# Performance work log

Hardware: AMD Instinct MI355X
Metric: run time of the kernel (lower is better)

The kernel has to match this reference:

```python
import jax, jax.numpy as jnp
import numpy as np

DEPTH, DIM, HEADS, MLP_HID, POS_DIM, PROJ_DIM, NCLS, INP = 5, 128, 8, 256, 128, 128, 1000, 35
EPS = 1e-5

def _ln(x, g, b):
    m = x.mean(-1, keepdims=True)
    v = ((x - m) ** 2).mean(-1, keepdims=True)
    return (x - m) / jnp.sqrt(v + EPS) * g + b

def _gelu(x):
    return jax.nn.gelu(x, approximate=False)  # torch nn.GELU default (erf)

def setup_inputs() -> dict:
    key = jax.random.key(0)
    ks = iter(jax.random.split(key, 80))
    nxt = lambda: next(ks)
    B, N = 8, 1024
    w = lambda *s: (jax.random.normal(nxt(), s, jnp.float32) / np.sqrt(s[-2]).astype(np.float32))
    z = lambda *s: jnp.zeros(s, jnp.float32)
    o = lambda *s: jnp.ones(s, jnp.float32)
    node_feat = jax.random.normal(nxt(), (B, N, 3), jnp.float32)
    a = (jax.random.uniform(nxt(), (B, N, N)) < 0.01).astype(jnp.float32)
    adj = jnp.maximum(a, a.transpose(0, 2, 1))  # symmetric 0/1 adjacency
    lapl = jax.random.normal(nxt(), (B, N, 32), jnp.float32) * 0.1
    d = dict(
        node_feat=node_feat, adj=adj, lapl=lapl,
        cls_token=jax.random.normal(nxt(), (1, 1, DIM), jnp.float32),
        pe_w1=w(INP, 2 * INP), pe_b1=z(2 * INP),
        pe_w2=w(2 * INP, 2 * INP), pe_b2=z(2 * INP),
        pe_w3=w(2 * INP, 2 * INP), pe_b3=z(2 * INP),
        pe_lng=o(2 * INP), pe_lnb=z(2 * INP),
        pe_w4=w(2 * INP, POS_DIM), pe_b4=z(POS_DIM),
        blk_ln1_g=o(DEPTH, DIM), blk_ln1_b=z(DEPTH, DIM),
        blk_qkv_w=w(DEPTH, DIM, 3 * HEADS * DIM),
        blk_proj_w=w(DEPTH, HEADS * DIM, DIM), blk_proj_b=z(DEPTH, DIM),
        blk_gamma_w=jax.random.uniform(nxt(), (DEPTH, DIM, 2), jnp.float32) * 0.01,
        blk_gamma_b=z(DEPTH, 2),
        blk_ln2_g=o(DEPTH, DIM), blk_ln2_b=z(DEPTH, DIM),
        blk_mlp_w1=w(DEPTH, DIM, MLP_HID), blk_mlp_b1=z(DEPTH, MLP_HID),
        blk_mlp_w2=w(DEPTH, MLP_HID, DIM), blk_mlp_b2=z(DEPTH, DIM),
        head_lng=o(DIM), head_lnb=z(DIM), head_w=w(DIM, DIM), head_b=z(DIM),
        proj_w1=w(DIM, PROJ_DIM), proj_b1=z(PROJ_DIM),
        proj_w2=w(PROJ_DIM, PROJ_DIM), proj_b2=z(PROJ_DIM),
        proj_w3=w(PROJ_DIM, PROJ_DIM), proj_b3=z(PROJ_DIM),
        proj_lng=o(PROJ_DIM), proj_lnb=z(PROJ_DIM),
        proj_w4=w(PROJ_DIM, NCLS), proj_b4=z(NCLS),
    )
    return d

def reference(node_feat, adj, lapl, cls_token, pe_w1, pe_b1, pe_w2, pe_b2, pe_w3, pe_b3,
              pe_lng, pe_lnb, pe_w4, pe_b4, blk_ln1_g, blk_ln1_b, blk_qkv_w, blk_proj_w,
              blk_proj_b, blk_gamma_w, blk_gamma_b, blk_ln2_g, blk_ln2_b, blk_mlp_w1,
              blk_mlp_b1, blk_mlp_w2, blk_mlp_b2, head_lng, head_lnb, head_w, head_b,
              proj_w1, proj_b1, proj_w2, proj_b2, proj_w3, proj_b3, proj_lng, proj_lnb,
              proj_w4, proj_b4):
    B, N, _ = node_feat.shape
    M = N + 1
    # positional-encoding MLP on concatenated [node_feat | lapl] (inp_dim = 35)
    x = jnp.concatenate([node_feat, lapl], axis=2)
    x = _gelu(x @ pe_w1 + pe_b1)
    x = _gelu(x @ pe_w2 + pe_b2)
    x = _gelu(x @ pe_w3 + pe_b3)
    x = _ln(x, pe_lng, pe_lnb) @ pe_w4 + pe_b4  # [B,N,DIM]
    x = jnp.concatenate([jnp.broadcast_to(cls_token, (B, 1, DIM)), x], axis=1)  # [B,M,DIM]
    # adjacency with cls row/col, adj_cls[:,0,0] = 1
    adj_cls = jnp.zeros((B, M, M), x.dtype).at[:, 0, 0].set(1.0).at[:, 1:, 1:].set(adj)
    scale = DIM ** (-0.5)
    for i in range(DEPTH):
        h = _ln(x, blk_ln1_g[i], blk_ln1_b[i])
        qkv = (h @ blk_qkv_w[i]).reshape(B, M, 3, HEADS, DIM).transpose(2, 0, 3, 1, 4)
        q, k, v = qkv[0], qkv[1], qkv[2]  # each [B,H,M,D]
        attn = jnp.einsum('bhnd,bhmd->bhnm', q, k) * scale
        gamma = jnp.exp(h @ blk_gamma_w[i] + blk_gamma_b[i])  # [B,M,2], use_exp=True
        attn = gamma[:, None, :, 0:1] * attn + gamma[:, None, :, 1:2] * adj_cls[:, None]
        attn = jax.nn.softmax(attn, axis=-1)
        o = jnp.einsum('bhnm,bhmd->bhnd', attn, v).transpose(0, 2, 1, 3).reshape(B, M, HEADS * DIM)
        x = o @ blk_proj_w[i] + blk_proj_b[i] + h  # residual from normed input (as in source)
        h2 = _ln(x, blk_ln2_g[i], blk_ln2_b[i])
        x = _gelu(h2 @ blk_mlp_w1[i] + blk_mlp_b1[i]) @ blk_mlp_w2[i] + blk_mlp_b2[i] + h2
    c = x[:, 0]
    c = _ln(c, head_lng, head_lnb) @ head_w + head_b  # mlp_head
    p = _gelu(c @ proj_w1 + proj_b1)
    p = _gelu(p @ proj_w2 + proj_b2)
    p = _gelu(p @ proj_w3 + proj_b3)
    p = _ln(p, proj_lng, proj_lnb) @ proj_w4 + proj_b4
    return (c, p)
```

## Files before the change

kernel.cpp:

```cpp
#include <hip/hip_runtime.h>
#include <hip/hip_bf16.h>
#include <math.h>

#define NB 8
#define NSEQ 1024
#define M_ 1025
#define ROWS (NB * M_)
#define DIMC 128
#define NHEADS 8
#define QKV3 3072
#define PEROWS (NB * NSEQ)
#define ACS 1088

typedef __attribute__((ext_vector_type(8))) short bf16x8;
typedef __attribute__((ext_vector_type(4))) float f32x4;

__device__ __forceinline__ float gelu_f(float x) {
  return 0.5f * x * (1.f + erff(x * 0.70710678118654752440f));
}

__device__ __forceinline__ unsigned short f2bf(float f) {
  __hip_bfloat16 h = __float2bfloat16(f);
  return *reinterpret_cast<unsigned short*>(&h);
}

__device__ __forceinline__ float bf2f(unsigned short u) {
  union { unsigned int i; float f; } c;
  c.i = ((unsigned int)u) << 16;
  return c.f;
}

template<int TR>
__global__ __launch_bounds__(256) void rowgemm_k(
    const float* __restrict__ in, const float* __restrict__ W,
    const float* __restrict__ bias, const float* __restrict__ res,
    float* __restrict__ out, int rows, int K, int Nout, int act, int remap)
{
  extern __shared__ float s_in[];
  const int tid = threadIdx.x;
  const int r0 = blockIdx.x * TR;
  const int tot = TR * K;
  for (int idx = tid; idx < tot; idx += blockDim.x) {
    int r = idx / K;
    int k = idx - r * K;
    int gr = r0 + r;
    s_in[idx] = (gr < rows) ? in[(size_t)gr * K + k] : 0.f;
  }
  __syncthreads();
  const int j = blockIdx.y * blockDim.x + tid;
  if (j >= Nout) return;
  float acc[TR];
  const float bv = bias ? bias[j] : 0.f;
#pragma unroll
  for (int r = 0; r < TR; ++r) acc[r] = bv;
  for (int k = 0; k < K; ++k) {
    const float w = W[(size_t)k * Nout + j];
#pragma unroll
    for (int r = 0; r < TR; ++r) acc[r] = fmaf(s_in[r * K + k], w, acc[r]);
  }
  for (int r = 0; r < TR; ++r) {
    const int gr = r0 + r;
    if (gr >= rows) break;
    float v = acc[r];
    if (act == 1) v = gelu_f(v);
    if (res) v += res[(size_t)gr * Nout + j];
    const size_t orow = remap ? (size_t)(gr + gr / 1024 + 1) : (size_t)gr;
    out[orow * (size_t)Nout + j] = v;
  }
}

template<int ACT, int OBF, int RES>
__global__ __launch_bounds__(256) void mgemm_k(
    const unsigned short* __restrict__ Xb, const unsigned short* __restrict__ Wt,
    const float* __restrict__ bias, const float* __restrict__ res,
    void* __restrict__ outp, int rows, int K, int N)
{
  __shared__ unsigned short sX[64][72];
  __shared__ unsigned short sW[64][72];
  const int tid = threadIdx.x;
  const int w = tid >> 6, lane = tid & 63;
  const int col = lane & 15, quad = lane >> 4;
  const int r0 = blockIdx.x * 64, n0 = blockIdx.y * 64;
  const int lr = tid >> 2, lc = tid & 3;
  const int xrow = min(r0 + lr, rows - 1);
  const unsigned short* xsrc = Xb + (size_t)xrow * K + lc * 8;
  const unsigned short* wsrc = Wt + (size_t)(n0 + lr) * K + lc * 8;

  f32x4 acc[4];
#pragma unroll
  for (int t = 0; t < 4; ++t) acc[t] = (f32x4){0.f, 0.f, 0.f, 0.f};

  for (int k0 = 0; k0 < K; k0 += 64) {
    __syncthreads();
    *(uint4*)&sX[lr][lc * 8]      = *(const uint4*)(xsrc + k0);
    *(uint4*)&sX[lr][lc * 8 + 32] = *(const uint4*)(xsrc + k0 + 32);
    *(uint4*)&sW[lr][lc * 8]      = *(const uint4*)(wsrc + k0);
    *(uint4*)&sW[lr][lc * 8 + 32] = *(const uint4*)(wsrc + k0 + 32);
    __syncthreads();
    const bf16x8 aX0 = *(const bf16x8*)&sX[w * 16 + col][quad * 8];
    const bf16x8 aX1 = *(const bf16x8*)&sX[w * 16 + col][32 + quad * 8];
#pragma unroll
    for (int t = 0; t < 4; ++t) {
      const bf16x8 bW0 = *(const bf16x8*)&sW[t * 16 + col][quad * 8];
      const bf16x8 bW1 = *(const bf16x8*)&sW[t * 16 + col][32 + quad * 8];
      acc[t] = __builtin_amdgcn_mfma_f32_16x16x32_bf16(aX0, bW0, acc[t], 0, 0, 0);
      acc[t] = __builtin_amdgcn_mfma_f32_16x16x32_bf16(aX1, bW1, acc[t], 0, 0, 0);
    }
  }
  const int gr_base = r0 + w * 16 + quad * 4;
#pragma unroll
  for (int t = 0; t < 4; ++t) {
    const int n = n0 + t * 16 + col;
    const float bv = bias ? bias[n] : 0.f;
#pragma unroll
    for (int r = 0; r < 4; ++r) {
      const int gr = gr_base + r;
      if (gr < rows) {
        float v = acc[t][r] + bv;
        if (ACT) v = gelu_f(v);
        if (RES) v += res[(size_t)gr * N + n];
        if (OBF) ((unsigned short*)outp)[(size_t)gr * N + n] = f2bf(v);
        else     ((float*)outp)[(size_t)gr * N + n] = v;
      }
    }
  }
}

template<int OBF>
__global__ __launch_bounds__(256) void mgemm128_k(
    const unsigned short* __restrict__ Xb, const unsigned short* __restrict__ Wt,
    const float* __restrict__ bias, void* __restrict__ outp,
    int rows, int K, int N)
{
  __shared__ unsigned short sX[128][72];
  __shared__ unsigned short sW[128][72];
  const int tid = threadIdx.x;
  const int w = tid >> 6, lane = tid & 63;
  const int col = lane & 15, quad = lane >> 4;
  const int wr = w >> 1, wc = w & 1;
  const int r0 = blockIdx.x * 128, n0 = blockIdx.y * 128;

  f32x4 acc[4][4];
#pragma unroll
  for (int i = 0; i < 4; ++i)
#pragma unroll
    for (int j = 0; j < 4; ++j) acc[i][j] = (f32x4){0.f, 0.f, 0.f, 0.f};

  for (int k0 = 0; k0 < K; k0 += 64) {
    __syncthreads();
#pragma unroll
    for (int l = 0; l < 4; ++l) {
      const int idx = l * 256 + tid;
      const int row = idx >> 3, c = idx & 7;
      const int xrow = min(r0 + row, rows - 1);
      *(uint4*)&sX[row][c * 8] = *(const uint4*)(Xb + (size_t)xrow * K + k0 + c * 8);
      *(uint4*)&sW[row][c * 8] = *(const uint4*)(Wt + (size_t)(n0 + row) * K + k0 + c * 8);
    }
    __syncthreads();
    bf16x8 aX[4][2];
#pragma unroll
    for (int i = 0; i < 4; ++i) {
      aX[i][0] = *(const bf16x8*)&sX[wr * 64 + i * 16 + col][quad * 8];
      aX[i][1] = *(const bf16x8*)&sX[wr * 64 + i * 16 + col][32 + quad * 8];
    }
#pragma unroll
    for (int j = 0; j < 4; ++j) {
      const bf16x8 b0 = *(const bf16x8*)&sW[wc * 64 + j * 16 + col][quad * 8];
      const bf16x8 b1 = *(const bf16x8*)&sW[wc * 64 + j * 16 + col][32 + quad * 8];
#pragma unroll
      for (int i = 0; i < 4; ++i) {
        acc[i][j] = __builtin_amdgcn_mfma_f32_16x16x32_bf16(aX[i][0], b0, acc[i][j], 0, 0, 0);
        acc[i][j] = __builtin_amdgcn_mfma_f32_16x16x32_bf16(aX[i][1], b1, acc[i][j], 0, 0, 0);
      }
    }
  }
#pragma unroll
  for (int i = 0; i < 4; ++i) {
    const int gr_base = r0 + wr * 64 + i * 16 + quad * 4;
#pragma unroll
    for (int j = 0; j < 4; ++j) {
      const int n = n0 + wc * 64 + j * 16 + col;
      const float bv = bias ? bias[n] : 0.f;
#pragma unroll
      for (int r = 0; r < 4; ++r) {
        const int gr = gr_base + r;
        if (gr < rows) {
          const float v = acc[i][j][r] + bv;
          if (OBF) ((unsigned short*)outp)[(size_t)gr * N + n] = f2bf(v);
          else     ((float*)outp)[(size_t)gr * N + n] = v;
        }
      }
    }
  }
}

__global__ __launch_bounds__(256) void ln_rows_k(
    const float* __restrict__ in, float* __restrict__ out,
    unsigned short* __restrict__ outb,
    const float* __restrict__ g, const float* __restrict__ b,
    const float* __restrict__ gw, const float* __restrict__ gb,
    float* __restrict__ gamout, int rows, int D)
{
  const int wv = (blockIdx.x * blockDim.x + threadIdx.x) >> 6;
  const int lane = threadIdx.x & 63;
  if (wv >= rows) return;
  const float* r = in + (size_t)wv * D;
  float s = 0.f;
  for (int d = lane; d < D; d += 64) s += r[d];
  for (int off = 32; off; off >>= 1) s += __shfl_down(s, off);
  const float mean = __shfl(s, 0) / (float)D;
  float v = 0.f;
  for (int d = lane; d < D; d += 64) { float t = r[d] - mean; v += t * t; }
  for (int off = 32; off; off >>= 1) v += __shfl_down(v, off);
  const float inv = rsqrtf(__shfl(v, 0) / (float)D + 1e-5f);
  float* orow = out + (size_t)wv * D;
  float a0 = 0.f, a1 = 0.f;
  for (int d = lane; d < D; d += 64) {
    const float o = (r[d] - mean) * inv * g[d] + b[d];
    orow[d] = o;
    if (outb) outb[(size_t)wv * D + d] = f2bf(o);
    if (gw) { a0 = fmaf(o, gw[2 * d], a0); a1 = fmaf(o, gw[2 * d + 1], a1); }
  }
  if (gw) {
    for (int off = 32; off; off >>= 1) { a0 += __shfl_down(a0, off); a1 += __shfl_down(a1, off); }
    if (lane == 0) {
      gamout[(size_t)wv * 2 + 0] = expf(a0 + gb[0]);
      gamout[(size_t)wv * 2 + 1] = expf(a1 + gb[1]);
    }
  }
}

__global__ __launch_bounds__(256) void adjp_k(const float* __restrict__ adj,
                                              unsigned long long* __restrict__ adjp)
{
  const int n = blockIdx.x;
  const int b = blockIdx.y;
  const int wv = threadIdx.x >> 6, lane = threadIdx.x & 63;
  for (int w = wv; w < 17; w += 4) {
    const int m = w * 64 + lane;
    float av = 0.f;
    if (n == 0) av = (m == 0) ? 1.f : 0.f;
    else if (m >= 1 && m <= NSEQ) av = adj[((size_t)b * NSEQ + (n - 1)) * NSEQ + (m - 1)];
    const unsigned long long mask = __ballot(av != 0.f);
    if (lane == 0) adjp[((size_t)b * M_ + n) * 17 + w] = mask;
  }
}

__global__ void wtrans_k(const float* __restrict__ W, unsigned short* __restrict__ Wt,
                         int K, int N)
{
  __shared__ float t[32][33];
  const int k0 = blockIdx.x * 32, n0 = blockIdx.y * 32;
  const float* Wd = W + (size_t)blockIdx.z * K * N;
  unsigned short* Wtd = Wt + (size_t)blockIdx.z * K * N;
  for (int i = threadIdx.y; i < 32; i += 8)
    t[i][threadIdx.x] = Wd[(size_t)(k0 + i) * N + n0 + threadIdx.x];
  __syncthreads();
  for (int i = threadIdx.y; i < 32; i += 8)
    Wtd[(size_t)(n0 + i) * K + k0 + threadIdx.x] = f2bf(t[threadIdx.x][i]);
}

__global__ __launch_bounds__(256) void vtrans_k(
    const unsigned short* __restrict__ qkv, unsigned short* __restrict__ vt)
{
  __shared__ unsigned short sT[64][136];
  const int mt = blockIdx.x, hh = blockIdx.y, b = blockIdx.z;
  const int tid = threadIdx.x;
  const int m0 = mt * 64;
#pragma unroll
  for (int l = 0; l < 4; ++l) {
    const int idx = l * 256 + tid;
    const int m = idx >> 4, c = idx & 15;
    const int gm = m0 + m;
    uint4 v = make_uint4(0u, 0u, 0u, 0u);
    if (gm < M_) v = *(const uint4*)(qkv + ((size_t)(b * M_ + gm)) * QKV3 + 2048 + hh * DIMC + c * 8);
    *(uint4*)&sT[m][c * 8] = v;
  }
  __syncthreads();
#pragma unroll
  for (int l = 0; l < 4; ++l) {
    const int idx = l * 256 + tid;
    const int d = idx >> 3, mc = idx & 7;
    unsigned short tmp[8];
#pragma unroll
    for (int j = 0; j < 8; ++j) tmp[j] = sT[mc * 8 + j][d];
    *(uint4*)(vt + (((size_t)(b * NHEADS + hh) * DIMC + d) * ACS) + m0 + mc * 8) = *(uint4*)tmp;
  }
}

__global__ __launch_bounds__(256) void attn_mfma_k(
    const unsigned short* __restrict__ qkv, const float* __restrict__ gamma,
    const unsigned long long* __restrict__ adjp, const unsigned short* __restrict__ vt,
    unsigned short* __restrict__ o)
{
  __shared__ unsigned short sK[64][136];
  __shared__ unsigned short sVt[128][72];
  __shared__ unsigned short sP[64][72];

  const int hh = blockIdx.x, qt = blockIdx.y, b = blockIdx.z;
  const int tid = threadIdx.x;
  const int w = tid >> 6;
  const int lane = tid & 63;
  const int col = lane & 15;
  const int quad = lane >> 4;
  const int n0 = qt * 64;
  const int qbase = n0 + w * 16;
  const float scale = 0.088388347648318447f;

  bf16x8 aQ[4];
  {
    const int qrow = min(qbase + col, 1024);
    const unsigned short* qp = qkv + ((size_t)(b * M_ + qrow)) * QKV3 + hh * DIMC + quad * 8;
#pragma unroll
    for (int c = 0; c < 4; ++c) aQ[c] = *(const bf16x8*)(qp + c * 32);
  }
  float g0[4], g1[4];
  size_t adjo[4];
#pragma unroll
  for (int r = 0; r < 4; ++r) {
    const int nc = min(qbase + quad * 4 + r, 1024);
    g0[r] = gamma[(size_t)(b * M_ + nc) * 2 + 0] * scale;
    g1[r] = gamma[(size_t)(b * M_ + nc) * 2 + 1];
    adjo[r] = ((size_t)b * M_ + nc) * 17;
  }

  float l_i[4] = {0.f, 0.f, 0.f, 0.f};
  f32x4 Oacc[8];
#pragma unroll
  for (int t = 0; t < 8; ++t) Oacc[t] = (f32x4){0.f, 0.f, 0.f, 0.f};

  const size_t vtbase = ((size_t)(b * NHEADS + hh)) * DIMC * ACS;

  for (int kt = 0; kt < 17; ++kt) {
    const int m0 = kt * 64;
    __syncthreads();
#pragma unroll
    for (int l = 0; l < 4; ++l) {
      const int idx = l * 256 + tid;
      {
        const int m = idx >> 4, c = idx & 15;
        const int gm = m0 + m;
        uint4 kv = make_uint4(0u, 0u, 0u, 0u);
        if (gm < M_) kv = *(const uint4*)(qkv + ((size_t)(b * M_ + gm)) * QKV3 + 1024 + hh * DIMC + c * 8);
        *(uint4*)&sK[m][c * 8] = kv;
      }
      {
        const int d = idx >> 3, mc = idx & 7;
        const uint4 vv = *(const uint4*)(vt + vtbase + (size_t)d * ACS + m0 + mc * 8);
        const int swc = mc ^ ((d >> 3) & 7);
        *(uint4*)&sVt[d][swc * 8] = vv;
      }
    }
    __syncthreads();

    unsigned long long mk[4];
#pragma unroll
    for (int r = 0; r < 4; ++r) mk[r] = adjp[adjo[r] + kt];

    f32x4 Sacc[4];
#pragma unroll
    for (int t = 0; t < 4; ++t) Sacc[t] = (f32x4){0.f, 0.f, 0.f, 0.f};
#pragma unroll
    for (int t = 0; t < 4; ++t) {
#pragma unroll
      for (int c = 0; c < 4; ++c) {
        const bf16x8 bK = *(const bf16x8*)&sK[t * 16 + col][c * 32 + quad * 8];
        Sacc[t] = __builtin_amdgcn_mfma_f32_16x16x32_bf16(aQ[c], bK, Sacc[t], 0, 0, 0);
      }
    }

#pragma unroll
    for (int t = 0; t < 4; ++t) {
      const int m = m0 + t * 16 + col;
      const bool mv = (m < M_);
      const int chb = t * 2 + (col >> 3);
      const int sh = t * 16 + col;
#pragma unroll
      for (int r = 0; r < 4; ++r) {
        const float bias = ((mk[r] >> sh) & 1ull) ? g1[r] : 0.f;
        const float s = fmaf(g0[r], Sacc[t][r], bias);
        const float pv = mv ? __expf(s) : 0.f;
        l_i[r] += pv;
        const int ql = w * 16 + quad * 4 + r;
        sP[ql][((chb ^ (ql & 7)) * 8) + (col & 7)] = f2bf(pv);
      }
    }

#pragma unroll
    for (int ch = 0; ch < 2; ++ch) {
      const int r0a = w * 16 + col;
      const bf16x8 aP = *(const bf16x8*)&sP[r0a][(((ch * 4 + quad) ^ (col & 7)) * 8)];
#pragma unroll
      for (int t = 0; t < 8; ++t) {
        const int pc = (ch * 4 + quad) ^ ((t * 2 + (col >> 3)) & 7);
        const bf16x8 bV = *(const bf16x8*)&sVt[t * 16 + col][pc * 8];
        Oacc[t] = __builtin_amdgcn_mfma_f32_16x16x32_bf16(aP, bV, Oacc[t], 0, 0, 0);
      }
    }
  }

#pragma unroll
  for (int r = 0; r < 4; ++r) {
    float s = l_i[r];
    s += __shfl_xor(s, 1);
    s += __shfl_xor(s, 2);
    s += __shfl_xor(s, 4);
    s += __shfl_xor(s, 8);
    const int n = qbase + quad * 4 + r;
    if (n < M_) {
      const float invl = 1.f / s;
      unsigned short* orow = o + ((size_t)(b * M_ + n)) * (NHEADS * DIMC) + hh * DIMC + col;
#pragma unroll
      for (int t = 0; t < 8; ++t) orow[t * 16] = f2bf(Oacc[t][r] * invl);
    }
  }
}

__global__ __launch_bounds__(256) void head_fused_k(
    const float* __restrict__ x,
    const float* __restrict__ hlg, const float* __restrict__ hlb,
    const float* __restrict__ hw, const float* __restrict__ hb,
    const float* __restrict__ pw1, const float* __restrict__ pb1,
    const float* __restrict__ pw2, const float* __restrict__ pb2,
    const float* __restrict__ pw3, const float* __restrict__ pb3,
    const float* __restrict__ plg, const float* __restrict__ plb,
    const float* __restrict__ pw4, const float* __restrict__ pb4,
    float* __restrict__ out_c, float* __restrict__ out_p)
{
  __shared__ float sA[8][128];
  __shared__ float sB[8][128];
  const int tid = threadIdx.x;

  for (int i = tid; i < 8 * 128; i += 256) {
    const int bb = i >> 7, d = i & 127;
    sA[bb][d] = x[(size_t)bb * M_ * DIMC + d];
  }
  __syncthreads();
  if (tid < 8) {
    float m = 0.f;
    for (int d = 0; d < 128; ++d) m += sA[tid][d];
    m *= (1.f / 128.f);
    float v = 0.f;
    for (int d = 0; d < 128; ++d) { const float t = sA[tid][d] - m; v += t * t; }
    const float inv = rsqrtf(v * (1.f / 128.f) + 1e-5f);
    for (int d = 0; d < 128; ++d) sA[tid][d] = (sA[tid][d] - m) * inv * hlg[d] + hlb[d];
  }
  __syncthreads();
  {
    const int j = tid & 127, rb = (tid >> 7) * 4;
    float acc[4];
#pragma unroll
    for (int r = 0; r < 4; ++r) acc[r] = hb[j];
    for (int k = 0; k < 128; ++k) {
      const float wv = hw[k * 128 + j];
#pragma unroll
      for (int r = 0; r < 4; ++r) acc[r] = fmaf(sA[rb + r][k], wv, acc[r]);
    }
#pragma unroll
    for (int r = 0; r < 4; ++r) { sB[rb + r][j] = acc[r]; out_c[(rb + r) * 128 + j] = acc[r]; }
  }
  __syncthreads();
  const float* Ws[3] = {pw1, pw2, pw3};
  const float* Bs[3] = {pb1, pb2, pb3};
  for (int s = 0; s < 3; ++s) {
    const float (*src)[128] = (s & 1) ? sA : sB;
    float (*dst)[128] = (s & 1) ? sB : sA;
    const int j = tid & 127, rb = (tid >> 7) * 4;
    float acc[4];
#pragma unroll
    for (int r = 0; r < 4; ++r) acc[r] = Bs[s][j];
    for (int k = 0; k < 128; ++k) {
      const float wv = Ws[s][k * 128 + j];
#pragma unroll
      for (int r = 0; r < 4; ++r) acc[r] = fmaf(src[rb + r][k], wv, acc[r]);
    }
#pragma unroll
    for (int r = 0; r < 4; ++r) dst[rb + r][j] = gelu_f(acc[r]);
    __syncthreads();
  }
  if (tid < 8) {
    float m = 0.f;
    for (int d = 0; d < 128; ++d) m += sA[tid][d];
    m *= (1.f / 128.f);
    float v = 0.f;
    for (int d = 0; d < 128; ++d) { const float t = sA[tid][d] - m; v += t * t; }
    const float inv = rsqrtf(v * (1.f / 128.f) + 1e-5f);
    for (int d = 0; d < 128; ++d) sA[tid][d] = (sA[tid][d] - m) * inv * plg[d] + plb[d];
  }
  __syncthreads();
  for (int j = tid; j < 1000; j += 256) {
    float acc[8];
#pragma unroll
    for (int bb = 0; bb < 8; ++bb) acc[bb] = pb4[j];
    for (int k = 0; k < 128; ++k) {
      const float wv = pw4[(size_t)k * 1000 + j];
#pragma unroll
      for (int bb = 0; bb < 8; ++bb) acc[bb] = fmaf(sA[bb][k], wv, acc[bb]);
    }
#pragma unroll
    for (int bb = 0; bb < 8; ++bb) out_p[bb * 1000 + j] = acc[bb];
  }
}

__global__ void concat_pe_k(const float* __restrict__ nf, const float* __restrict__ lp,
                            float* __restrict__ x35, int rows)
{
  const int idx = blockIdx.x * blockDim.x + threadIdx.x;
  if (idx >= rows * 35) return;
  const int r = idx / 35, c = idx - r * 35;
  x35[idx] = (c < 3) ? nf[(size_t)r * 3 + c] : lp[(size_t)r * 32 + (c - 3)];
}

__global__ void fill_cls_k(const float* __restrict__ cls, float* __restrict__ x)
{
  x[(size_t)blockIdx.x * M_ * DIMC + threadIdx.x] = cls[threadIdx.x];
}

extern "C" void kernel_launch(void* const* d_in, const int* in_sizes, int n_in,
                              void* d_out, int out_size, void* d_ws, size_t ws_size,
                              hipStream_t stream)
{
  (void)in_sizes; (void)n_in; (void)out_size; (void)ws_size;
  const float* node_feat = (const float*)d_in[0];
  const float* adj       = (const float*)d_in[1];
  const float* lapl      = (const float*)d_in[2];
  const float* cls_token = (const float*)d_in[3];
  const float* pe_w1 = (const float*)d_in[4];
  const float* pe_b1 = (const float*)d_in[5];
  const float* pe_w2 = (const float*)d_in[6];
  const float* pe_b2 = (const float*)d_in[7];
  const float* pe_w3 = (const float*)d_in[8];
  const float* pe_b3 = (const float*)d_in[9];
  const float* pe_lng = (const float*)d_in[10];
  const float* pe_lnb = (const float*)d_in[11];
  const float* pe_w4 = (const float*)d_in[12];
  const float* pe_b4 = (const float*)d_in[13];
  const float* blk_ln1_g = (const float*)d_in[14];
  const float* blk_ln1_b = (const float*)d_in[15];
  const float* blk_qkv_w = (const float*)d_in[16];
  const float* blk_proj_w = (const float*)d_in[17];
  const float* blk_proj_b = (const float*)d_in[18];
  const float* blk_gamma_w = (const float*)d_in[19];
  const float* blk_gamma_b = (const float*)d_in[20];
  const float* blk_ln2_g = (const float*)d_in[21];
  const float* blk_ln2_b = (const float*)d_in[22];
  const float* blk_mlp_w1 = (const float*)d_in[23];
  const float* blk_mlp_b1 = (const float*)d_in[24];
  const float* blk_mlp_w2 = (const float*)d_in[25];
  const float* blk_mlp_b2 = (const float*)d_in[26];
  const float* head_lng = (const float*)d_in[27];
  const float* head_lnb = (const float*)d_in[28];
  const float* head_w = (const float*)d_in[29];
  const float* head_b = (const float*)d_in[30];
  const float* proj_w1 = (const float*)d_in[31];
  const float* proj_b1 = (const float*)d_in[32];
  const float* proj_w2 = (const float*)d_in[33];
  const float* proj_b2 = (const float*)d_in[34];
  const float* proj_w3 = (const float*)d_in[35];
  const float* proj_b3 = (const float*)d_in[36];
  const float* proj_lng = (const float*)d_in[37];
  const float* proj_lnb = (const float*)d_in[38];
  const float* proj_w4 = (const float*)d_in[39];
  const float* proj_b4 = (const float*)d_in[40];

  float* ws   = (float*)d_ws;
  float* x    = ws;
  float* h    = x + 1049600;
  float* gam  = h + 1049600;
  float* obuf = gam + 16400;
  unsigned short* obufb = (unsigned short*)obuf;
  unsigned short* hidb  = (unsigned short*)(obuf + 4198400);
  float* x35 = obuf;
  float* xa  = obuf + 300000;
  float* xb  = obuf + 900000;
  float* sm  = obuf + 5248000;
  unsigned short* hb   = (unsigned short*)(sm + 8192);
  unsigned short* qkv  = hb + 1049600;
  unsigned long long* adjp = (unsigned long long*)(qkv + 25190400);
  unsigned short* vt   = (unsigned short*)(adjp + 139400 + 88);
  unsigned short* qkvWt = vt + 8912896;
  unsigned short* projWt = qkvWt + 5 * 393216;
  unsigned short* mlp1Wt = projWt + 5 * 131072;
  unsigned short* mlp2Wt = mlp1Wt + 5 * 32768;

  float* out_c = (float*)d_out;
  float* out_p = out_c + NB * DIMC;

  adjp_k<<<dim3(M_, NB), 256, 0, stream>>>(adj, adjp);
  wtrans_k<<<dim3(4, 96, 5), dim3(32, 8), 0, stream>>>(blk_qkv_w, qkvWt, 128, 3072);
  wtrans_k<<<dim3(32, 4, 5), dim3(32, 8), 0, stream>>>(blk_proj_w, projWt, 1024, 128);
  wtrans_k<<<dim3(4, 8, 5), dim3(32, 8), 0, stream>>>(blk_mlp_w1, mlp1Wt, 128, 256);
  wtrans_k<<<dim3(8, 4, 5), dim3(32, 8), 0, stream>>>(blk_mlp_w2, mlp2Wt, 256, 128);

  concat_pe_k<<<(PEROWS * 35 + 255) / 256, 256, 0, stream>>>(node_feat, lapl, x35, PEROWS);
  rowgemm_k<16><<<dim3(512, 1), 128, 16 * 35 * 4, stream>>>(x35, pe_w1, pe_b1, nullptr, xa, PEROWS, 35, 70, 1, 0);
  rowgemm_k<16><<<dim3(512, 1), 128, 16 * 70 * 4, stream>>>(xa, pe_w2, pe_b2, nullptr, xb, PEROWS, 70, 70, 1, 0);
  rowgemm_k<16><<<dim3(512, 1), 128, 16 * 70 * 4, stream>>>(xb, pe_w3, pe_b3, nullptr, xa, PEROWS, 70, 70, 1, 0);
  ln_rows_k<<<(PEROWS * 64 + 255) / 256, 256, 0, stream>>>(xa, xb, nullptr, pe_lng, pe_lnb, nullptr, nullptr, nullptr, PEROWS, 70);
  rowgemm_k<16><<<dim3(512, 1), 128, 16 * 70 * 4, stream>>>(xb, pe_w4, pe_b4, nullptr, x, PEROWS, 70, DIMC, 0, 1);
  fill_cls_k<<<NB, DIMC, 0, stream>>>(cls_token, x);

  const int lnGrid = (ROWS * 64 + 255) / 256;
  for (int i = 0; i < 5; ++i) {
    const float* ln1g = blk_ln1_g + i * DIMC;
    const float* ln1b = blk_ln1_b + i * DIMC;
    const float* pb   = blk_proj_b + i * DIMC;
    const float* gw   = blk_gamma_w + (size_t)i * DIMC * 2;
    const float* gb   = blk_gamma_b + i * 2;
    const float* ln2g = blk_ln2_g + i * DIMC;
    const float* ln2b = blk_ln2_b + i * DIMC;
    const float* mb1  = blk_mlp_b1 + i * 256;
    const float* mb2  = blk_mlp_b2 + i * DIMC;
    const unsigned short* qw = qkvWt + (size_t)i * 393216;
    const unsigned short* pw = projWt + (size_t)i * 131072;
    const unsigned short* m1w = mlp1Wt + (size_t)i * 32768;
    const unsigned short* m2w = mlp2Wt + (size_t)i * 32768;

    ln_rows_k<<<lnGrid, 256, 0, stream>>>(x, h, hb, ln1g, ln1b, gw, gb, gam, ROWS, DIMC);
    mgemm128_k<1><<<dim3(65, 24), 256, 0, stream>>>(hb, qw, nullptr, qkv, ROWS, 128, 3072);
    vtrans_k<<<dim3(17, NHEADS, NB), 256, 0, stream>>>(qkv, vt);
    attn_mfma_k<<<dim3(NHEADS, 17, NB), 256, 0, stream>>>(qkv, gam, adjp, vt, obufb);
    mgemm_k<0, 0, 1><<<dim3(129, 2), 256, 0, stream>>>(obufb, pw, pb, h, x, ROWS, 1024, 128);
    ln_rows_k<<<lnGrid, 256, 0, stream>>>(x, h, hb, ln2g, ln2b, nullptr, nullptr, nullptr, ROWS, DIMC);
    mgemm_k<1, 1, 0><<<dim3(129, 4), 256, 0, stream>>>(hb, m1w, mb1, nullptr, hidb, ROWS, 128, 256);
    mgemm_k<0, 0, 1><<<dim3(129, 2), 256, 0, stream>>>(hidb, m2w, mb2, h, x, ROWS, 256, 128);
  }

  head_fused_k<<<1, 256, 0, stream>>>(x, head_lng, head_lnb, head_w, head_b,
                                      proj_w1, proj_b1, proj_w2, proj_b2,
                                      proj_w3, proj_b3, proj_lng, proj_lnb,
                                      proj_w4, proj_b4, out_c, out_p);
}
```

Measured before the change: 1.625 ms.

## Fuse positional-encoding MLP into one kernel and write V-transpose from QKV GEMM

The concat, three GELU linears, LayerNorm and final linear of the positional-encoding MLP now run in a single kernel. Intermediates stay in shared memory, which removes five launches and the global round trips between them. The separate V-transpose kernel is gone: the QKV GEMM epilogue scatters the V columns directly into the transposed vt layout as bf16. Those scattered 2-byte stores are strided by ACS and poorly coalesced. Unlike the old kernel, padded rows past 1025 are no longer zero-filled.

```diff
diff --git a/kernel.cpp b/kernel.cpp
--- a/kernel.cpp
+++ b/kernel.cpp
@@ -30,42 +30,90 @@
   return c.f;
 }
 
-template<int TR>
-__global__ __launch_bounds__(256) void rowgemm_k(
-    const float* __restrict__ in, const float* __restrict__ W,
-    const float* __restrict__ bias, const float* __restrict__ res,
-    float* __restrict__ out, int rows, int K, int Nout, int act, int remap)
-{
-  extern __shared__ float s_in[];
+__global__ __launch_bounds__(128) void pe_fused_k(
+    const float* __restrict__ nf, const float* __restrict__ lp,
+    const float* __restrict__ w1, const float* __restrict__ b1,
+    const float* __restrict__ w2, const float* __restrict__ b2,
+    const float* __restrict__ w3, const float* __restrict__ b3,
+    const float* __restrict__ lng, const float* __restrict__ lnb,
+    const float* __restrict__ w4, const float* __restrict__ b4,
+    float* __restrict__ x)
+{
+  __shared__ float sA[16][36];
+  __shared__ float sB[16][72];
+  __shared__ float sC[16][72];
   const int tid = threadIdx.x;
-  const int r0 = blockIdx.x * TR;
-  const int tot = TR * K;
-  for (int idx = tid; idx < tot; idx += blockDim.x) {
-    int r = idx / K;
-    int k = idx - r * K;
-    int gr = r0 + r;
-    s_in[idx] = (gr < rows) ? in[(size_t)gr * K + k] : 0.f;
-  }
-  __syncthreads();
-  const int j = blockIdx.y * blockDim.x + tid;
-  if (j >= Nout) return;
-  float acc[TR];
-  const float bv = bias ? bias[j] : 0.f;
-#pragma unroll
-  for (int r = 0; r < TR; ++r) acc[r] = bv;
-  for (int k = 0; k < K; ++k) {
-    const float w = W[(size_t)k * Nout + j];
-#pragma unroll
-    for (int r = 0; r < TR; ++r) acc[r] = fmaf(s_in[r * K + k], w, acc[r]);
-  }
-  for (int r = 0; r < TR; ++r) {
+  const int r0 = blockIdx.x * 16;
+
+  for (int i = tid; i < 16 * 35; i += 128) {
+    const int r = i / 35, c = i - r * 35;
     const int gr = r0 + r;
-    if (gr >= rows) break;
-    float v = acc[r];
-    if (act == 1) v = gelu_f(v);
-    if (res) v += res[(size_t)gr * Nout + j];
-    const size_t orow = remap ? (size_t)(gr + gr / 1024 + 1) : (size_t)gr;
-    out[orow * (size_t)Nout + j] = v;
+    sA[r][c] = (c < 3) ? nf[(size_t)gr * 3 + c] : lp[(size_t)gr * 32 + (c - 3)];
+  }
+  __syncthreads();
+  if (tid < 70) {
+    float acc[16];
+#pragma unroll
+    for (int r = 0; r < 16; ++r) acc[r] = b1[tid];
+    for (int k = 0; k < 35; ++k) {
+      const float wv = w1[k * 70 + tid];
+#pragma unroll
+      for (int r = 0; r < 16; ++r) acc[r] = fmaf(sA[r][k], wv, acc[r]);
+    }
+#pragma unroll
+    for (int r = 0; r < 16; ++r) sB[r][tid] = gelu_f(acc[r]);
+  }
+  __syncthreads();
+  if (tid < 70) {
+    float acc[16];
+#pragma unroll
+    for (int r = 0; r < 16; ++r) acc[r] = b2[tid];
+    for (int k = 0; k < 70; ++k) {
+      const float wv = w2[k * 70 + tid];
+#pragma unroll
+      for (int r = 0; r < 16; ++r) acc[r] = fmaf(sB[r][k], wv, acc[r]);
+    }
+#pragma unroll
+    for (int r = 0; r < 16; ++r) sC[r][tid] = gelu_f(acc[r]);
+  }
+  __syncthreads();
+  if (tid < 70) {
+    float acc[16];
+#pragma unroll
+    for (int r = 0; r < 16; ++r) acc[r] = b3[tid];
+    for (int k = 0; k < 70; ++k) {
+      const float wv = w3[k * 70 + tid];
+#pragma unroll
+      for (int r = 0; r < 16; ++r) acc[r] = fmaf(sC[r][k], wv, acc[r]);
+    }
+#pragma unroll
+    for (int r = 0; r < 16; ++r) sB[r][tid] = gelu_f(acc[r]);
+  }
+  __syncthreads();
+  if (tid < 16) {
+    float m = 0.f;
+    for (int d = 0; d < 70; ++d) m += sB[tid][d];
+    m *= (1.f / 70.f);
+    float v = 0.f;
+    for (int d = 0; d < 70; ++d) { const float t = sB[tid][d] - m; v += t * t; }
+    const float inv = rsqrtf(v * (1.f / 70.f) + 1e-5f);
+    for (int d = 0; d < 70; ++d) sB[tid][d] = (sB[tid][d] - m) * inv * lng[d] + lnb[d];
+  }
+  __syncthreads();
+  {
+    float acc[16];
+#pragma unroll
+    for (int r = 0; r < 16; ++r) acc[r] = b4[tid];
+    for (int k = 0; k < 70; ++k) {
+      const float wv = w4[k * 128 + tid];
+#pragma unroll
+      for (int r = 0; r < 16; ++r) acc[r] = fmaf(sB[r][k], wv, acc[r]);
+    }
+#pragma unroll
+    for (int r = 0; r < 16; ++r) {
+      const int gr = r0 + r;
+      x[(size_t)(gr + gr / 1024 + 1) * DIMC + tid] = acc[r];
+    }
   }
 }
 
@@ -126,11 +174,11 @@
   }
 }
 
-template<int OBF>
+template<int OBF, int VT>
 __global__ __launch_bounds__(256) void mgemm128_k(
     const unsigned short* __restrict__ Xb, const unsigned short* __restrict__ Wt,
     const float* __restrict__ bias, void* __restrict__ outp,
-    int rows, int K, int N)
+    unsigned short* __restrict__ vtp, int rows, int K, int N)
 {
   __shared__ unsigned short sX[128][72];
   __shared__ unsigned short sW[128][72];
@@ -174,20 +222,34 @@
       }
     }
   }
+  const bool dovt = VT && (n0 >= 2048);
 #pragma unroll
   for (int i = 0; i < 4; ++i) {
     const int gr_base = r0 + wr * 64 + i * 16 + quad * 4;
+    int bb[4], mm[4];
+    if (dovt) {
+#pragma unroll
+      for (int r = 0; r < 4; ++r) {
+        const int gr = gr_base + r;
+        bb[r] = gr / 1025;
+        mm[r] = gr - bb[r] * 1025;
+      }
+    }
 #pragma unroll
     for (int j = 0; j < 4; ++j) {
       const int n = n0 + wc * 64 + j * 16 + col;
       const float bv = bias ? bias[n] : 0.f;
+      const int hh = (n - 2048) >> 7;
+      const int d  = (n - 2048) & 127;
 #pragma unroll
       for (int r = 0; r < 4; ++r) {
         const int gr = gr_base + r;
         if (gr < rows) {
           const float v = acc[i][j][r] + bv;
-          if (OBF) ((unsigned short*)outp)[(size_t)gr * N + n] = f2bf(v);
+          const unsigned short bf = f2bf(v);
+          if (OBF) ((unsigned short*)outp)[(size_t)gr * N + n] = bf;
           else     ((float*)outp)[(size_t)gr * N + n] = v;
+          if (dovt) vtp[(((size_t)(bb[r] * NHEADS + hh) * DIMC + d) * ACS) + mm[r]] = bf;
         }
       }
     }
@@ -260,34 +322,6 @@
     Wtd[(size_t)(n0 + i) * K + k0 + threadIdx.x] = f2bf(t[threadIdx.x][i]);
 }
 
-__global__ __launch_bounds__(256) void vtrans_k(
-    const unsigned short* __restrict__ qkv, unsigned short* __restrict__ vt)
-{
-  __shared__ unsigned short sT[64][136];
-  const int mt = blockIdx.x, hh = blockIdx.y, b = blockIdx.z;
-  const int tid = threadIdx.x;
-  const int m0 = mt * 64;
-#pragma unroll
-  for (int l = 0; l < 4; ++l) {
-    const int idx = l * 256 + tid;
-    const int m = idx >> 4, c = idx & 15;
-    const int gm = m0 + m;
-    uint4 v = make_uint4(0u, 0u, 0u, 0u);
-    if (gm < M_) v = *(const uint4*)(qkv + ((size_t)(b * M_ + gm)) * QKV3 + 2048 + hh * DIMC + c * 8);
-    *(uint4*)&sT[m][c * 8] = v;
-  }
-  __syncthreads();
-#pragma unroll
-  for (int l = 0; l < 4; ++l) {
-    const int idx = l * 256 + tid;
-    const int d = idx >> 3, mc = idx & 7;
-    unsigned short tmp[8];
-#pragma unroll
-    for (int j = 0; j < 8; ++j) tmp[j] = sT[mc * 8 + j][d];
-    *(uint4*)(vt + (((size_t)(b * NHEADS + hh) * DIMC + d) * ACS) + m0 + mc * 8) = *(uint4*)tmp;
-  }
-}
-
 __global__ __launch_bounds__(256) void attn_mfma_k(
     const unsigned short* __restrict__ qkv, const float* __restrict__ gamma,
     const unsigned long long* __restrict__ adjp, const unsigned short* __restrict__ vt,
@@ -500,15 +534,6 @@
 #pragma unroll
     for (int bb = 0; bb < 8; ++bb) out_p[bb * 1000 + j] = acc[bb];
   }
-}
-
-__global__ void concat_pe_k(const float* __restrict__ nf, const float* __restrict__ lp,
-                            float* __restrict__ x35, int rows)
-{
-  const int idx = blockIdx.x * blockDim.x + threadIdx.x;
-  if (idx >= rows * 35) return;
-  const int r = idx / 35, c = idx - r * 35;
-  x35[idx] = (c < 3) ? nf[(size_t)r * 3 + c] : lp[(size_t)r * 32 + (c - 3)];
 }
 
 __global__ void fill_cls_k(const float* __restrict__ cls, float* __restrict__ x)
@@ -570,9 +595,6 @@
   float* obuf = gam + 16400;
   unsigned short* obufb = (unsigned short*)obuf;
   unsigned short* hidb  = (unsigned short*)(obuf + 4198400);
-  float* x35 = obuf;
-  float* xa  = obuf + 300000;
-  float* xb  = obuf + 900000;
   float* sm  = obuf + 5248000;
   unsigned short* hb   = (unsigned short*)(sm + 8192);
   unsigned short* qkv  = hb + 1049600;
@@ -592,12 +614,8 @@
   wtrans_k<<<dim3(4, 8, 5), dim3(32, 8), 0, stream>>>(blk_mlp_w1, mlp1Wt, 128, 256);
   wtrans_k<<<dim3(8, 4, 5), dim3(32, 8), 0, stream>>>(blk_mlp_w2, mlp2Wt, 256, 128);
 
-  concat_pe_k<<<(PEROWS * 35 + 255) / 256, 256, 0, stream>>>(node_feat, lapl, x35, PEROWS);
-  rowgemm_k<16><<<dim3(512, 1), 128, 16 * 35 * 4, stream>>>(x35, pe_w1, pe_b1, nullptr, xa, PEROWS, 35, 70, 1, 0);
-  rowgemm_k<16><<<dim3(512, 1), 128, 16 * 70 * 4, stream>>>(xa, pe_w2, pe_b2, nullptr, xb, PEROWS, 70, 70, 1, 0);
-  rowgemm_k<16><<<dim3(512, 1), 128, 16 * 70 * 4, stream>>>(xb, pe_w3, pe_b3, nullptr, xa, PEROWS, 70, 70, 1, 0);
-  ln_rows_k<<<(PEROWS * 64 + 255) / 256, 256, 0, stream>>>(xa, xb, nullptr, pe_lng, pe_lnb, nullptr, nullptr, nullptr, PEROWS, 70);
-  rowgemm_k<16><<<dim3(512, 1), 128, 16 * 70 * 4, stream>>>(xb, pe_w4, pe_b4, nullptr, x, PEROWS, 70, DIMC, 0, 1);
+  pe_fused_k<<<512, 128, 0, stream>>>(node_feat, lapl, pe_w1, pe_b1, pe_w2, pe_b2,
+                                      pe_w3, pe_b3, pe_lng, pe_lnb, pe_w4, pe_b4, x);
   fill_cls_k<<<NB, DIMC, 0, stream>>>(cls_token, x);
 
   const int lnGrid = (ROWS * 64 + 255) / 256;
@@ -617,8 +635,7 @@
     const unsigned short* m2w = mlp2Wt + (size_t)i * 32768;
 
     ln_rows_k<<<lnGrid, 256, 0, stream>>>(x, h, hb, ln1g, ln1b, gw, gb, gam, ROWS, DIMC);
-    mgemm128_k<1><<<dim3(65, 24), 256, 0, stream>>>(hb, qw, nullptr, qkv, ROWS, 128, 3072);
-    vtrans_k<<<dim3(17, NHEADS, NB), 256, 0, stream>>>(qkv, vt);
+    mgemm128_k<1, 1><<<dim3(65, 24), 256, 0, stream>>>(hb, qw, nullptr, qkv, vt, ROWS, 128, 3072);
     attn_mfma_k<<<dim3(NHEADS, 17, NB), 256, 0, stream>>>(qkv, gam, adjp, vt, obufb);
     mgemm_k<0, 0, 1><<<dim3(129, 2), 256, 0, stream>>>(obufb, pw, pb, h, x, ROWS, 1024, 128);
     ln_rows_k<<<lnGrid, 256, 0, stream>>>(x, h, hb, ln2g, ln2b, nullptr, nullptr, nullptr, ROWS, DIMC);
```

New measurement: 1.593 ms (median of 2 runs). No clear change (-2.0%).
